# Optimization experiments

Measured on AMD Instinct MI355X. Metric: run time of the kernel, lower is better.

Reference implementation:

```python
import jax, jax.numpy as jnp
import numpy as np

BS, H, W = 4, 64, 64
NG, NP = 2, 192          # prim groups per class, points per group
SCORING_WEIGHT = 0.01


def setup_inputs() -> dict:
    key = jax.random.key(0)
    ks = jax.random.split(key, 6)
    pred_r = jax.random.normal(ks[0], (BS, 4, H, W), jnp.float32)
    pred_t = jax.random.normal(ks[1], (BS, 3, H, W), jnp.float32)
    # scores must be positive (log(ps) in the loss)
    pred_s = jax.random.uniform(ks[2], (BS, 1, H, W), jnp.float32, 0.05, 1.0)
    gt_r = jax.random.normal(ks[3], (BS, 3, 3), jnp.float32)
    gt_t = jax.random.normal(ks[4], (BS, 3), jnp.float32)
    grps = jax.random.normal(ks[5], (NG, 3, NP), jnp.float32)
    mask = jnp.ones((BS, 1, H, W), jnp.float32)  # all-valid -> static stride selection
    cls_ids = jnp.zeros((BS,), jnp.int32)        # single class; grps are its prim groups
    return dict(pred_r=pred_r, pred_t=pred_t, pred_s=pred_s, gt_r=gt_r,
                gt_t=gt_t, grps=grps, mask=mask, cls_ids=cls_ids, step=20)


def quat_to_mat(pr):
    # pr: [bs, 4, n] (unit quaternions); exact layout from the torch source
    q0, q1, q2, q3 = pr[:, 0], pr[:, 1], pr[:, 2], pr[:, 3]
    R = jnp.stack([
        1.0 - 2.0 * (q2 ** 2 + q3 ** 2), 2.0 * q1 * q2 - 2.0 * q0 * q3, 2.0 * q0 * q2 + 2.0 * q1 * q3,
        2.0 * q1 * q2 + 2.0 * q3 * q0, 1.0 - 2.0 * (q1 ** 2 + q3 ** 2), -2.0 * q0 * q1 + 2.0 * q2 * q3,
        -2.0 * q0 * q2 + 2.0 * q1 * q3, 2.0 * q0 * q1 + 2.0 * q2 * q3, 1.0 - 2.0 * (q1 ** 2 + q2 ** 2),
    ], axis=-1)                                  # [bs, n, 9]
    return R.reshape(R.shape[0], R.shape[1], 3, 3)


def reference(pred_r, pred_t, pred_s, gt_r, gt_t, grps, mask, cls_ids, step):
    bs, _, h, w = pred_r.shape
    hw = h * w
    # normalize quaternion channels per pixel
    pred_r = pred_r / jnp.linalg.norm(pred_r, axis=1, keepdims=True)
    pred_r = pred_r.reshape(bs, 4, hw)
    pred_t = pred_t.reshape(bs, 3, hw)
    ps_all = pred_s.reshape(bs, hw)
    # mask is all-ones (see setup), so valid-pixel subsampling is a static stride
    nv = hw // step
    idx = jnp.arange(nv) * step
    pr = pred_r[:, :, idx]                       # [bs,4,nv]
    pt = pred_t[:, :, idx]                       # [bs,3,nv]
    ps = ps_all[:, idx]                          # [bs,nv]
    R_pre = quat_to_mat(pr)                      # [bs,nv,3,3]
    # predicted points: rotate each group by the per-pixel R, add per-pixel t
    P = jnp.einsum('bnij,gjp->bgnip', R_pre, grps) \
        + pt.transpose(0, 2, 1)[:, None, :, :, None]     # [bs,g,nv,3,np]
    # target points: gt pose applied to each group (shared across pixels)
    T = jnp.einsum('bij,gjp->bgip', gt_r, grps) + gt_t[:, None, :, None]  # [bs,g,3,np]
    # pairwise euclidean distances via gemm identity (avoids [.,np,np,3] blowup)
    cross = jnp.einsum('bgit,bgnip->bgntp', T, P)        # [bs,g,nv,np_t,np_p]
    t2 = jnp.sum(T * T, axis=2)[:, :, None, :, None]
    p2 = jnp.sum(P * P, axis=3)[:, :, :, None, :]
    dist = jnp.sqrt(jnp.maximum(t2 + p2 - 2.0 * cross, 1e-12))
    # for each target point, nearest predicted point (one-directional chamfer)
    min_dist = jnp.min(dist, axis=-1)            # [bs,g,nv,np_t]
    add_ij = jnp.mean(min_dist, axis=-1)         # [bs,g,nv]
    # NG == 2 -> the mean-over-groups branch of the original
    add_i = jnp.mean(add_ij, axis=1)             # [bs,nv]
    loss_lst = jnp.mean(add_i * ps - SCORING_WEIGHT * jnp.log(ps), axis=1)  # [bs]
    loss = jnp.mean(loss_lst)
    return loss
```

## Files before the change

### kernel.cpp

```cpp
#include <hip/hip_runtime.h>

#define HW    4096
#define STEP  20
#define NV    204
#define NPNT  192
#define NGRP  2
#define BSZ   4
#define SCORING_WEIGHT 0.01f
#define NBLK  (BSZ * NGRP * NV)

__global__ __launch_bounds__(192) void k_dist(
    const float* __restrict__ pred_r,
    const float* __restrict__ pred_t,
    const float* __restrict__ gt_r,
    const float* __restrict__ gt_t,
    const float* __restrict__ grps,
    float* __restrict__ partial)
{
    __shared__ float ssq[NPNT];
    __shared__ float wsum[3];

    const int blk = blockIdx.x;
    const int n   = blk % NV;
    const int g   = (blk / NV) % NGRP;
    const int b   = blk / (NV * NGRP);
    const int pix = n * STEP;
    const int tid = threadIdx.x;

    const float* __restrict__ G0 = grps + g * 3 * NPNT;
    const float* __restrict__ G1 = G0 + NPNT;
    const float* __restrict__ G2 = G0 + 2 * NPNT;

    const float a0 = G0[tid];
    const float a1 = G1[tid];
    const float a2 = G2[tid];
    ssq[tid] = a0 * a0 + a1 * a1 + a2 * a2;

    float q0 = pred_r[(b * 4 + 0) * HW + pix];
    float q1 = pred_r[(b * 4 + 1) * HW + pix];
    float q2 = pred_r[(b * 4 + 2) * HW + pix];
    float q3 = pred_r[(b * 4 + 3) * HW + pix];
    {
        float inv = 1.0f / sqrtf(q0 * q0 + q1 * q1 + q2 * q2 + q3 * q3);
        q0 *= inv; q1 *= inv; q2 *= inv; q3 *= inv;
    }
    const float R00 = 1.f - 2.f * (q2 * q2 + q3 * q3);
    const float R01 = 2.f * q1 * q2 - 2.f * q0 * q3;
    const float R02 = 2.f * q0 * q2 + 2.f * q1 * q3;
    const float R10 = 2.f * q1 * q2 + 2.f * q3 * q0;
    const float R11 = 1.f - 2.f * (q1 * q1 + q3 * q3);
    const float R12 = -2.f * q0 * q1 + 2.f * q2 * q3;
    const float R20 = -2.f * q0 * q2 + 2.f * q1 * q3;
    const float R21 = 2.f * q0 * q1 + 2.f * q2 * q3;
    const float R22 = 1.f - 2.f * (q1 * q1 + q2 * q2);

    const float pt0 = pred_t[(b * 3 + 0) * HW + pix];
    const float pt1 = pred_t[(b * 3 + 1) * HW + pix];
    const float pt2 = pred_t[(b * 3 + 2) * HW + pix];

    const float* Rb = gt_r + b * 9;
    const float* tb = gt_t + b * 3;
    const float T0 = Rb[0] * a0 + Rb[1] * a1 + Rb[2] * a2 + tb[0];
    const float T1 = Rb[3] * a0 + Rb[4] * a1 + Rb[5] * a2 + tb[1];
    const float T2 = Rb[6] * a0 + Rb[7] * a1 + Rb[8] * a2 + tb[2];
    const float u0 = T0 - pt0;
    const float u1 = T1 - pt1;
    const float u2 = T2 - pt2;
    const float V0 = R00 * u0 + R10 * u1 + R20 * u2;
    const float V1 = R01 * u0 + R11 * u1 + R21 * u2;
    const float V2 = R02 * u0 + R12 * u1 + R22 * u2;
    const float Vsq = V0 * V0 + V1 * V1 + V2 * V2;

    __syncthreads();

    const float4* __restrict__ G0v = reinterpret_cast<const float4*>(G0);
    const float4* __restrict__ G1v = reinterpret_cast<const float4*>(G1);
    const float4* __restrict__ G2v = reinterpret_cast<const float4*>(G2);
    const float4* __restrict__ SQv = reinterpret_cast<const float4*>(ssq);
    float mm0 = 3.4e38f, mm1 = 3.4e38f, mm2 = 3.4e38f, mm3 = 3.4e38f;
#pragma unroll
    for (int p4 = 0; p4 < NPNT / 4; ++p4) {
        const float4 x = G0v[p4];
        const float4 y = G1v[p4];
        const float4 z = G2v[p4];
        const float4 sq = SQv[p4];
        {
            const float dot = fmaf(V2, z.x, fmaf(V1, y.x, V0 * x.x));
            mm0 = fminf(mm0, fmaf(-2.f, dot, sq.x));
        }
        {
            const float dot = fmaf(V2, z.y, fmaf(V1, y.y, V0 * x.y));
            mm1 = fminf(mm1, fmaf(-2.f, dot, sq.y));
        }
        {
            const float dot = fmaf(V2, z.z, fmaf(V1, y.z, V0 * x.z));
            mm2 = fminf(mm2, fmaf(-2.f, dot, sq.z));
        }
        {
            const float dot = fmaf(V2, z.w, fmaf(V1, y.w, V0 * x.w));
            mm3 = fminf(mm3, fmaf(-2.f, dot, sq.w));
        }
    }
    const float m = fminf(fminf(mm0, mm1), fminf(mm2, mm3));
    const float dist = sqrtf(fmaxf(Vsq + m, 1e-12f));

    float s = dist;
    for (int off = 32; off > 0; off >>= 1) s += __shfl_down(s, off);
    const int wid  = tid >> 6;
    const int lane = tid & 63;
    if (lane == 0) wsum[wid] = s;
    __syncthreads();
    if (tid == 0) partial[blk] = wsum[0] + wsum[1] + wsum[2];
}

__global__ __launch_bounds__(256) void k_reduce(
    const float* __restrict__ partial,
    const float* __restrict__ pred_s,
    float* __restrict__ out)
{
    __shared__ float redA[256];
    __shared__ float redB[256];
    const int tid = threadIdx.x;

    float acc = 0.f;
    for (int k = tid; k < NBLK; k += 256) {
        const int n = k % NV;
        const int b = k / (NV * NGRP);
        const float ps = pred_s[b * HW + n * STEP];
        acc += partial[k] * ps;
    }
    float acc2 = 0.f;
    for (int k = tid; k < BSZ * NV; k += 256) {
        const int n = k % NV;
        const int b = k / NV;
        acc2 += logf(pred_s[b * HW + n * STEP]);
    }
    redA[tid] = acc;
    redB[tid] = acc2;
    __syncthreads();
    for (int s = 128; s > 0; s >>= 1) {
        if (tid < s) { redA[tid] += redA[tid + s]; redB[tid] += redB[tid + s]; }
        __syncthreads();
    }
    if (tid == 0) {
        const float sum_w  = redA[0] / (float)(NGRP * NPNT);
        const float sum_lg = redB[0];
        out[0] = (sum_w - SCORING_WEIGHT * sum_lg) / (float)(BSZ * NV);
    }
}

extern "C" void kernel_launch(void* const* d_in, const int* in_sizes, int n_in,
                              void* d_out, int out_size, void* d_ws, size_t ws_size,
                              hipStream_t stream) {
    const float* pred_r = (const float*)d_in[0];
    const float* pred_t = (const float*)d_in[1];
    const float* pred_s = (const float*)d_in[2];
    const float* gt_r   = (const float*)d_in[3];
    const float* gt_t   = (const float*)d_in[4];
    const float* grps   = (const float*)d_in[5];
    float* out     = (float*)d_out;
    float* partial = (float*)d_ws;

    k_dist<<<NBLK, 192, 0, stream>>>(pred_r, pred_t, gt_r, gt_t, grps, partial);
    k_reduce<<<1, 256, 0, stream>>>(partial, pred_s, out);
}
```

Before: 18.48 us.

## Process three pixels per block to reuse group point loads

Each block now handles three sampled pixels (n0, n0+68, n0+136) instead of one, so each loaded group point and squared norm feeds three distance evaluations. The grid shrinks from 1632 to 544 blocks. The -2 factor is folded into the per-pixel rotated vector so each candidate costs three FMAs plus a min. The trade-off is more registers and fewer blocks, which on a large GPU may reduce parallelism and latency hiding.

```diff
diff --git a/kernel.cpp b/kernel.cpp
--- a/kernel.cpp
+++ b/kernel.cpp
@@ -3,6 +3,7 @@
 #define HW    4096
 #define STEP  20
 #define NV    204
+#define NB0   68
 #define NPNT  192
 #define NGRP  2
 #define BSZ   4
@@ -18,13 +19,12 @@
     float* __restrict__ partial)
 {
     __shared__ float ssq[NPNT];
-    __shared__ float wsum[3];
+    __shared__ float wsum[3][3];
 
     const int blk = blockIdx.x;
-    const int n   = blk % NV;
-    const int g   = (blk / NV) % NGRP;
-    const int b   = blk / (NV * NGRP);
-    const int pix = n * STEP;
+    const int n0  = blk % NB0;
+    const int g   = (blk / NB0) % NGRP;
+    const int b   = blk / (NB0 * NGRP);
     const int tid = threadIdx.x;
 
     const float* __restrict__ G0 = grps + g * 3 * NPNT;
@@ -36,81 +36,91 @@
     const float a2 = G2[tid];
     ssq[tid] = a0 * a0 + a1 * a1 + a2 * a2;
 
-    float q0 = pred_r[(b * 4 + 0) * HW + pix];
-    float q1 = pred_r[(b * 4 + 1) * HW + pix];
-    float q2 = pred_r[(b * 4 + 2) * HW + pix];
-    float q3 = pred_r[(b * 4 + 3) * HW + pix];
-    {
-        float inv = 1.0f / sqrtf(q0 * q0 + q1 * q1 + q2 * q2 + q3 * q3);
-        q0 *= inv; q1 *= inv; q2 *= inv; q3 *= inv;
-    }
-    const float R00 = 1.f - 2.f * (q2 * q2 + q3 * q3);
-    const float R01 = 2.f * q1 * q2 - 2.f * q0 * q3;
-    const float R02 = 2.f * q0 * q2 + 2.f * q1 * q3;
-    const float R10 = 2.f * q1 * q2 + 2.f * q3 * q0;
-    const float R11 = 1.f - 2.f * (q1 * q1 + q3 * q3);
-    const float R12 = -2.f * q0 * q1 + 2.f * q2 * q3;
-    const float R20 = -2.f * q0 * q2 + 2.f * q1 * q3;
-    const float R21 = 2.f * q0 * q1 + 2.f * q2 * q3;
-    const float R22 = 1.f - 2.f * (q1 * q1 + q2 * q2);
-
-    const float pt0 = pred_t[(b * 3 + 0) * HW + pix];
-    const float pt1 = pred_t[(b * 3 + 1) * HW + pix];
-    const float pt2 = pred_t[(b * 3 + 2) * HW + pix];
-
     const float* Rb = gt_r + b * 9;
     const float* tb = gt_t + b * 3;
     const float T0 = Rb[0] * a0 + Rb[1] * a1 + Rb[2] * a2 + tb[0];
     const float T1 = Rb[3] * a0 + Rb[4] * a1 + Rb[5] * a2 + tb[1];
     const float T2 = Rb[6] * a0 + Rb[7] * a1 + Rb[8] * a2 + tb[2];
-    const float u0 = T0 - pt0;
-    const float u1 = T1 - pt1;
-    const float u2 = T2 - pt2;
-    const float V0 = R00 * u0 + R10 * u1 + R20 * u2;
-    const float V1 = R01 * u0 + R11 * u1 + R21 * u2;
-    const float V2 = R02 * u0 + R12 * u1 + R22 * u2;
-    const float Vsq = V0 * V0 + V1 * V1 + V2 * V2;
 
+    float W[3][3], Vsq[3];
+#pragma unroll
+    for (int j = 0; j < 3; ++j) {
+        const int pix = (n0 + NB0 * j) * STEP;
+        float q0 = pred_r[(b * 4 + 0) * HW + pix];
+        float q1 = pred_r[(b * 4 + 1) * HW + pix];
+        float q2 = pred_r[(b * 4 + 2) * HW + pix];
+        float q3 = pred_r[(b * 4 + 3) * HW + pix];
+        {
+            float inv = 1.0f / sqrtf(q0 * q0 + q1 * q1 + q2 * q2 + q3 * q3);
+            q0 *= inv; q1 *= inv; q2 *= inv; q3 *= inv;
+        }
+        const float R00 = 1.f - 2.f * (q2 * q2 + q3 * q3);
+        const float R01 = 2.f * q1 * q2 - 2.f * q0 * q3;
+        const float R02 = 2.f * q0 * q2 + 2.f * q1 * q3;
+        const float R10 = 2.f * q1 * q2 + 2.f * q3 * q0;
+        const float R11 = 1.f - 2.f * (q1 * q1 + q3 * q3);
+        const float R12 = -2.f * q0 * q1 + 2.f * q2 * q3;
+        const float R20 = -2.f * q0 * q2 + 2.f * q1 * q3;
+        const float R21 = 2.f * q0 * q1 + 2.f * q2 * q3;
+        const float R22 = 1.f - 2.f * (q1 * q1 + q2 * q2);
+
+        const float u0 = T0 - pred_t[(b * 3 + 0) * HW + pix];
+        const float u1 = T1 - pred_t[(b * 3 + 1) * HW + pix];
+        const float u2 = T2 - pred_t[(b * 3 + 2) * HW + pix];
+        const float V0 = R00 * u0 + R10 * u1 + R20 * u2;
+        const float V1 = R01 * u0 + R11 * u1 + R21 * u2;
+        const float V2 = R02 * u0 + R12 * u1 + R22 * u2;
+        Vsq[j]  = V0 * V0 + V1 * V1 + V2 * V2;
+        W[j][0] = -2.f * V0;
+        W[j][1] = -2.f * V1;
+        W[j][2] = -2.f * V2;
+    }
     __syncthreads();
 
     const float4* __restrict__ G0v = reinterpret_cast<const float4*>(G0);
     const float4* __restrict__ G1v = reinterpret_cast<const float4*>(G1);
     const float4* __restrict__ G2v = reinterpret_cast<const float4*>(G2);
     const float4* __restrict__ SQv = reinterpret_cast<const float4*>(ssq);
-    float mm0 = 3.4e38f, mm1 = 3.4e38f, mm2 = 3.4e38f, mm3 = 3.4e38f;
+    float mn[3][4];
 #pragma unroll
+    for (int j = 0; j < 3; ++j)
+#pragma unroll
+        for (int c = 0; c < 4; ++c) mn[j][c] = 3.4e38f;
+
+#pragma unroll 8
     for (int p4 = 0; p4 < NPNT / 4; ++p4) {
-        const float4 x = G0v[p4];
-        const float4 y = G1v[p4];
-        const float4 z = G2v[p4];
+        const float4 x  = G0v[p4];
+        const float4 y  = G1v[p4];
+        const float4 z  = G2v[p4];
         const float4 sq = SQv[p4];
-        {
-            const float dot = fmaf(V2, z.x, fmaf(V1, y.x, V0 * x.x));
-            mm0 = fminf(mm0, fmaf(-2.f, dot, sq.x));
-        }
-        {
-            const float dot = fmaf(V2, z.y, fmaf(V1, y.y, V0 * x.y));
-            mm1 = fminf(mm1, fmaf(-2.f, dot, sq.y));
-        }
-        {
-            const float dot = fmaf(V2, z.z, fmaf(V1, y.z, V0 * x.z));
-            mm2 = fminf(mm2, fmaf(-2.f, dot, sq.z));
-        }
-        {
-            const float dot = fmaf(V2, z.w, fmaf(V1, y.w, V0 * x.w));
-            mm3 = fminf(mm3, fmaf(-2.f, dot, sq.w));
+#pragma unroll
+        for (int j = 0; j < 3; ++j) {
+            const float w0 = W[j][0], w1 = W[j][1], w2 = W[j][2];
+            mn[j][0] = fminf(mn[j][0], fmaf(w2, z.x, fmaf(w1, y.x, fmaf(w0, x.x, sq.x))));
+            mn[j][1] = fminf(mn[j][1], fmaf(w2, z.y, fmaf(w1, y.y, fmaf(w0, x.y, sq.y))));
+            mn[j][2] = fminf(mn[j][2], fmaf(w2, z.z, fmaf(w1, y.z, fmaf(w0, x.z, sq.z))));
+            mn[j][3] = fminf(mn[j][3], fmaf(w2, z.w, fmaf(w1, y.w, fmaf(w0, x.w, sq.w))));
         }
     }
-    const float m = fminf(fminf(mm0, mm1), fminf(mm2, mm3));
-    const float dist = sqrtf(fmaxf(Vsq + m, 1e-12f));
 
-    float s = dist;
-    for (int off = 32; off > 0; off >>= 1) s += __shfl_down(s, off);
+    float s[3];
+#pragma unroll
+    for (int j = 0; j < 3; ++j) {
+        const float m = fminf(fminf(mn[j][0], mn[j][1]), fminf(mn[j][2], mn[j][3]));
+        s[j] = sqrtf(fmaxf(Vsq[j] + m, 1e-12f));
+    }
+    for (int off = 32; off > 0; off >>= 1) {
+        s[0] += __shfl_down(s[0], off);
+        s[1] += __shfl_down(s[1], off);
+        s[2] += __shfl_down(s[2], off);
+    }
     const int wid  = tid >> 6;
     const int lane = tid & 63;
-    if (lane == 0) wsum[wid] = s;
+    if (lane == 0) { wsum[0][wid] = s[0]; wsum[1][wid] = s[1]; wsum[2][wid] = s[2]; }
     __syncthreads();
-    if (tid == 0) partial[blk] = wsum[0] + wsum[1] + wsum[2];
+    if (tid < 3)
+        partial[(b * NGRP + g) * NV + n0 + NB0 * tid] =
+            wsum[tid][0] + wsum[tid][1] + wsum[tid][2];
 }
 
 __global__ __launch_bounds__(256) void k_reduce(
@@ -138,8 +148,8 @@
     redA[tid] = acc;
     redB[tid] = acc2;
     __syncthreads();
-    for (int s = 128; s > 0; s >>= 1) {
-        if (tid < s) { redA[tid] += redA[tid + s]; redB[tid] += redB[tid + s]; }
+    for (int st = 128; st > 0; st >>= 1) {
+        if (tid < st) { redA[tid] += redA[tid + st]; redB[tid] += redB[tid + st]; }
         __syncthreads();
     }
     if (tid == 0) {
@@ -161,6 +171,7 @@
     float* out     = (float*)d_out;
     float* partial = (float*)d_ws;
 
-    k_dist<<<NBLK, 192, 0, stream>>>(pred_r, pred_t, gt_r, gt_t, grps, partial);
+    k_dist<<<BSZ * NGRP * NB0, 192, 0, stream>>>(
+        pred_r, pred_t, gt_r, gt_t, grps, partial);
     k_reduce<<<1, 256, 0, stream>>>(partial, pred_s, out);
 }
```

Result: slower. 23.03 us (+24.6%).

## Split predicted-point scan across two thread halves and fold -2 into FMAs

Applied to the files above, without the earlier changes.

Each block now launches 384 threads: two halves each scan half of the predicted points for the same target point, then combine their minima through shared memory before the sqrt and warp reduction. The -2 scale is folded into the per-thread weights, so each point costs three FMAs plus a min. The goal is to shorten the serial inner loop and raise the number of waves in flight. In exchange it recomputes the per-thread setup in both halves and adds an extra barrier and shared-memory exchange.

```diff
diff --git a/kernel.cpp b/kernel.cpp
--- a/kernel.cpp
+++ b/kernel.cpp
@@ -8,8 +8,9 @@
 #define BSZ   4
 #define SCORING_WEIGHT 0.01f
 #define NBLK  (BSZ * NGRP * NV)
+#define NPH   (NPNT / 2 / 4)
 
-__global__ __launch_bounds__(192) void k_dist(
+__global__ __launch_bounds__(384, 8) void k_dist(
     const float* __restrict__ pred_r,
     const float* __restrict__ pred_t,
     const float* __restrict__ gt_r,
@@ -18,6 +19,7 @@
     float* __restrict__ partial)
 {
     __shared__ float ssq[NPNT];
+    __shared__ float m2[NPNT];
     __shared__ float wsum[3];
 
     const int blk = blockIdx.x;
@@ -26,15 +28,17 @@
     const int b   = blk / (NV * NGRP);
     const int pix = n * STEP;
     const int tid = threadIdx.x;
+    const int half = tid / NPNT;
+    const int t    = tid - half * NPNT;
 
     const float* __restrict__ G0 = grps + g * 3 * NPNT;
     const float* __restrict__ G1 = G0 + NPNT;
     const float* __restrict__ G2 = G0 + 2 * NPNT;
 
-    const float a0 = G0[tid];
-    const float a1 = G1[tid];
-    const float a2 = G2[tid];
-    ssq[tid] = a0 * a0 + a1 * a1 + a2 * a2;
+    const float a0 = G0[t];
+    const float a1 = G1[t];
+    const float a2 = G2[t];
+    if (half == 0) ssq[t] = a0 * a0 + a1 * a1 + a2 * a2;
 
     float q0 = pred_r[(b * 4 + 0) * HW + pix];
     float q1 = pred_r[(b * 4 + 1) * HW + pix];
@@ -70,45 +74,38 @@
     const float V1 = R01 * u0 + R11 * u1 + R21 * u2;
     const float V2 = R02 * u0 + R12 * u1 + R22 * u2;
     const float Vsq = V0 * V0 + V1 * V1 + V2 * V2;
+    const float w0 = -2.f * V0, w1 = -2.f * V1, w2 = -2.f * V2;
 
     __syncthreads();
 
-    const float4* __restrict__ G0v = reinterpret_cast<const float4*>(G0);
-    const float4* __restrict__ G1v = reinterpret_cast<const float4*>(G1);
-    const float4* __restrict__ G2v = reinterpret_cast<const float4*>(G2);
-    const float4* __restrict__ SQv = reinterpret_cast<const float4*>(ssq);
+    const int hbase = __builtin_amdgcn_readfirstlane(half * NPH);
+    const float4* __restrict__ G0v = reinterpret_cast<const float4*>(G0) + hbase;
+    const float4* __restrict__ G1v = reinterpret_cast<const float4*>(G1) + hbase;
+    const float4* __restrict__ G2v = reinterpret_cast<const float4*>(G2) + hbase;
+    const float4* __restrict__ SQv = reinterpret_cast<const float4*>(ssq) + hbase;
+
     float mm0 = 3.4e38f, mm1 = 3.4e38f, mm2 = 3.4e38f, mm3 = 3.4e38f;
-#pragma unroll
-    for (int p4 = 0; p4 < NPNT / 4; ++p4) {
-        const float4 x = G0v[p4];
-        const float4 y = G1v[p4];
-        const float4 z = G2v[p4];
+#pragma unroll 8
+    for (int p4 = 0; p4 < NPH; ++p4) {
+        const float4 x  = G0v[p4];
+        const float4 y  = G1v[p4];
+        const float4 z  = G2v[p4];
         const float4 sq = SQv[p4];
-        {
-            const float dot = fmaf(V2, z.x, fmaf(V1, y.x, V0 * x.x));
-            mm0 = fminf(mm0, fmaf(-2.f, dot, sq.x));
-        }
-        {
-            const float dot = fmaf(V2, z.y, fmaf(V1, y.y, V0 * x.y));
-            mm1 = fminf(mm1, fmaf(-2.f, dot, sq.y));
-        }
-        {
-            const float dot = fmaf(V2, z.z, fmaf(V1, y.z, V0 * x.z));
-            mm2 = fminf(mm2, fmaf(-2.f, dot, sq.z));
-        }
-        {
-            const float dot = fmaf(V2, z.w, fmaf(V1, y.w, V0 * x.w));
-            mm3 = fminf(mm3, fmaf(-2.f, dot, sq.w));
-        }
+        mm0 = fminf(mm0, fmaf(w2, z.x, fmaf(w1, y.x, fmaf(w0, x.x, sq.x))));
+        mm1 = fminf(mm1, fmaf(w2, z.y, fmaf(w1, y.y, fmaf(w0, x.y, sq.y))));
+        mm2 = fminf(mm2, fmaf(w2, z.z, fmaf(w1, y.z, fmaf(w0, x.z, sq.z))));
+        mm3 = fminf(mm3, fmaf(w2, z.w, fmaf(w1, y.w, fmaf(w0, x.w, sq.w))));
     }
-    const float m = fminf(fminf(mm0, mm1), fminf(mm2, mm3));
-    const float dist = sqrtf(fmaxf(Vsq + m, 1e-12f));
+    float m = fminf(fminf(mm0, mm1), fminf(mm2, mm3));
 
-    float s = dist;
-    for (int off = 32; off > 0; off >>= 1) s += __shfl_down(s, off);
-    const int wid  = tid >> 6;
-    const int lane = tid & 63;
-    if (lane == 0) wsum[wid] = s;
+    if (half == 1) m2[t] = m;
+    __syncthreads();
+    if (half == 0) {
+        m = fminf(m, m2[t]);
+        float s = sqrtf(fmaxf(Vsq + m, 1e-12f));
+        for (int off = 32; off > 0; off >>= 1) s += __shfl_down(s, off);
+        if ((t & 63) == 0) wsum[t >> 6] = s;
+    }
     __syncthreads();
     if (tid == 0) partial[blk] = wsum[0] + wsum[1] + wsum[2];
 }
@@ -138,8 +135,8 @@
     redA[tid] = acc;
     redB[tid] = acc2;
     __syncthreads();
-    for (int s = 128; s > 0; s >>= 1) {
-        if (tid < s) { redA[tid] += redA[tid + s]; redB[tid] += redB[tid + s]; }
+    for (int st = 128; st > 0; st >>= 1) {
+        if (tid < st) { redA[tid] += redA[tid + st]; redB[tid] += redB[tid + st]; }
         __syncthreads();
     }
     if (tid == 0) {
@@ -161,6 +158,6 @@
     float* out     = (float*)d_out;
     float* partial = (float*)d_ws;
 
-    k_dist<<<NBLK, 192, 0, stream>>>(pred_r, pred_t, gt_r, gt_t, grps, partial);
+    k_dist<<<NBLK, 384, 0, stream>>>(pred_r, pred_t, gt_r, gt_t, grps, partial);
     k_reduce<<<1, 256, 0, stream>>>(partial, pred_s, out);
 }
```

Measured after the change: 20.26 us. 1.1x slower.
